# Kernel optimization log

Hardware: AMD Instinct MI355X
Metric: run time of the kernel (lower is better)

## Reference

```python
import jax, jax.numpy as jnp
import numpy as np

DIM = 768
N_HEADS = 12
HEAD_DIM = DIM // N_HEADS
MLP_DIM = 3072
DEPTH = 12
B, N = 16, 512


def setup_inputs() -> dict:
    key = jax.random.key(0)
    ks = jax.random.split(key, 12)
    s = 0.02
    return {
        "x": jax.random.normal(ks[0], (B, N, DIM), dtype=jnp.float32),
        "ln_w": jnp.ones((DIM,), jnp.float32),
        "ln_b": jnp.zeros((DIM,), jnp.float32),
        "wq": jax.random.normal(ks[1], (DIM, DIM), jnp.float32) * s,
        "bq": jnp.zeros((DIM,), jnp.float32),
        "wk": jax.random.normal(ks[2], (DIM, DIM), jnp.float32) * s,
        "bk": jnp.zeros((DIM,), jnp.float32),
        "wv": jax.random.normal(ks[3], (DIM, DIM), jnp.float32) * s,
        "bv": jnp.zeros((DIM,), jnp.float32),
        "w1": jax.random.normal(ks[4], (DIM, MLP_DIM), jnp.float32) * s,
        "b1": jnp.zeros((MLP_DIM,), jnp.float32),
        "w2": jax.random.normal(ks[5], (MLP_DIM, DIM), jnp.float32) * s,
        "b2": jnp.zeros((DIM,), jnp.float32),
    }


def _layernorm(x, w, b):
    mu = jnp.mean(x, axis=-1, keepdims=True)
    var = jnp.var(x, axis=-1, keepdims=True)
    return (x - mu) * jax.lax.rsqrt(var + 1e-5) * w + b


def _mha(x, wq, bq, wk, bk, wv, bv):
    # x: [b, n, dim]; weights stored as [in, out]
    def heads(t):
        return t.reshape(B, N, N_HEADS, HEAD_DIM).transpose(0, 2, 1, 3)  # b h n d
    q = heads(x @ wq + bq)
    k = heads(x @ wk + bk)
    v = heads(x @ wv + bv)
    scores = jnp.einsum('bhqd,bhkd->bhqk', q, k) / np.sqrt(HEAD_DIM).astype(np.float32)
    attn = jax.nn.softmax(scores, axis=-1)
    o = jnp.einsum('bhqk,bhkd->bhqd', attn, v)
    return o.transpose(0, 2, 1, 3).reshape(B, N, DIM)


def reference(x, ln_w, ln_b, wq, bq, wk, bk, wv, bv, w1, b1, w2, b2):
    # Dropout is identity in eval mode. Same weights reused each depth iteration.
    for _ in range(DEPTH):
        x = _mha(_layernorm(x, ln_w, ln_b), wq, bq, wk, bk, wv, bv) + x
        h = _layernorm(x, ln_w, ln_b)
        h = jax.nn.gelu(h @ w1 + b1, approximate=False) @ w2 + b2
        x = h + x
    return x
```

## Files before the change

kernel.cpp:

```cpp
#include <hip/hip_runtime.h>

typedef __bf16 bf16x8 __attribute__((ext_vector_type(8)));
typedef float f32x4 __attribute__((ext_vector_type(4)));
typedef unsigned short ushort8_t __attribute__((ext_vector_type(8)));
typedef unsigned short ushort4_t __attribute__((ext_vector_type(4)));

#define MFMA16(a, b, c) __builtin_amdgcn_mfma_f32_16x16x32_bf16((a), (b), (c), 0, 0, 0)

#define GLOAD16(gp, lp)                                                        \
  __builtin_amdgcn_global_load_lds(                                            \
      (__attribute__((address_space(1))) void*)(gp),                           \
      (__attribute__((address_space(3))) void*)(lp), 16, 0, 0)

__device__ __forceinline__ unsigned short f2bf(float f) {
  unsigned u = __builtin_bit_cast(unsigned, f);
  return (unsigned short)((u + 0x7FFFu + ((u >> 16) & 1u)) >> 16);
}


__global__ __launch_bounds__(256) void transpose_f2b_tiled(
    const float* __restrict__ src, unsigned short* __restrict__ dst,
    int Kdim, int Ndim) {
  const long u = (long)blockIdx.x * 256 + threadIdx.x;
  const long total = ((long)Kdim * Ndim) >> 3;
  if (u >= total) return;
  const int kt32 = Kdim >> 5;
  const long tile = u >> 6;
  const int t8 = (int)(u & 63);
  const int chunk = t8 >> 4, rowlow = t8 & 15;
  const int n = (int)(tile / kt32) * 16 + rowlow;
  const int k0 = (int)(tile % kt32) * 32 + chunk * 8;
  ushort8_t o;
#pragma unroll
  for (int e = 0; e < 8; e++) o[e] = f2bf(src[(long)(k0 + e) * Ndim + n]);
  *(ushort8_t*)(dst + (u << 3)) = o;
}

__global__ __launch_bounds__(256) void ln_kernel(
    const float* __restrict__ x, const float* __restrict__ gw,
    const float* __restrict__ gb, unsigned short* __restrict__ h) {
  const int row = blockIdx.x * 4 + (threadIdx.x >> 6);
  const int l = threadIdx.x & 63;
  const float* xr = x + (long)row * 768;
  f32x4 va[3];
#pragma unroll
  for (int i = 0; i < 3; i++) va[i] = *(const f32x4*)(xr + i * 256 + l * 4);
  float s = 0.f, ss = 0.f;
#pragma unroll
  for (int i = 0; i < 3; i++)
#pragma unroll
    for (int j = 0; j < 4; j++) {
      float t = va[i][j];
      s += t;
      ss += t * t;
    }
#pragma unroll
  for (int off = 1; off < 64; off <<= 1) {
    s += __shfl_xor(s, off, 64);
    ss += __shfl_xor(ss, off, 64);
  }
  const float mu = s * (1.f / 768.f);
  const float var = ss * (1.f / 768.f) - mu * mu;
  const float inv = rsqrtf(var + 1e-5f);
  const long tb = ((long)(row >> 4) * 24) << 9;
  const int rlow = (row & 15) * 8;
  const int coff = ((l >> 1) & 3) * 128 + rlow + (l & 1) * 4;
#pragma unroll
  for (int i = 0; i < 3; i++) {
    f32x4 wv = *(const f32x4*)(gw + i * 256 + l * 4);
    f32x4 bv = *(const f32x4*)(gb + i * 256 + l * 4);
    ushort4_t o;
#pragma unroll
    for (int j = 0; j < 4; j++) o[j] = f2bf((va[i][j] - mu) * inv * wv[j] + bv[j]);
    const long addr = tb + ((long)(i * 8 + (l >> 3)) << 9) + coff;
    *(ushort4_t*)(h + addr) = o;
  }
}

enum { EPI_QKV = 0, EPI_GELU = 1, EPI_RES = 2 };

template <int EPI, int MREP>
__global__ __launch_bounds__(256) void gemm_bt(
    const unsigned short* __restrict__ A, const unsigned short* __restrict__ BT,
    int K, const float* __restrict__ bb0, const float* __restrict__ bb1,
    const float* __restrict__ bb2, unsigned short* __restrict__ o0,
    unsigned short* __restrict__ o1, unsigned short* __restrict__ o2,
    const float* oFin, float* oFout) {
  constexpr int BM = MREP * 32;
  constexpr int AG = BM / 16;
  __shared__ unsigned short As[2][2][AG * 512];
  __shared__ unsigned short Bs[2][2][8 * 512];
  const int tid = threadIdx.x;
  const int w = tid >> 6, l = tid & 63;
  const int lr = l & 15, lg = l >> 4;
  const int wr = w >> 1, wc = w & 1;

  const int nx = gridDim.x;
  const int nwg = nx * gridDim.y;
  int wg = blockIdx.y * nx + blockIdx.x;
  {
    const int qq = nwg >> 3, rr = nwg & 7;
    const int xcd = wg & 7, idx = wg >> 3;
    wg = (xcd < rr ? xcd * (qq + 1) : rr * (qq + 1) + (xcd - rr) * qq) + idx;
  }
  const int bx = wg % nx, by = wg / nx;
  const int m0 = by * BM, n0 = bx * 128;

  const int nk32 = K >> 5;
  const long abase = (long)(m0 >> 4) * nk32;
  const long bbase = (long)(n0 >> 4) * nk32;

  auto stage = [&](int buf, int kt) {
#pragma unroll
    for (int kk = 0; kk < 2; kk++) {
      const int pk = kt * 2 + kk;
#pragma unroll
      for (int t = 0; t < AG / 4; t++) {
        const int g = w + t * 4;
        GLOAD16(A + ((abase + (long)g * nk32 + pk) << 9) + l * 8,
                &As[buf][kk][g * 512 + l * 8]);
      }
#pragma unroll
      for (int t = 0; t < 2; t++) {
        const int g = w + t * 4;
        GLOAD16(BT + ((bbase + (long)g * nk32 + pk) << 9) + l * 8,
                &Bs[buf][kk][g * 512 + l * 8]);
      }
    }
  };

  f32x4 acc[MREP][4] = {};
  const int nk = K >> 6;
  stage(0, 0);
  for (int kt = 0; kt < nk; ++kt) {
    const int cur = kt & 1;
    __syncthreads();
    if (kt + 1 < nk) stage(cur ^ 1, kt + 1);
#pragma unroll
    for (int kk = 0; kk < 2; kk++) {
      bf16x8 a[MREP], b[4];
#pragma unroll
      for (int i = 0; i < MREP; i++)
        a[i] = *(const bf16x8*)(&As[cur][kk][(wr * MREP + i) * 512 + l * 8]);
#pragma unroll
      for (int j = 0; j < 4; j++)
        b[j] = *(const bf16x8*)(&Bs[cur][kk][(wc * 4 + j) * 512 + l * 8]);
      __builtin_amdgcn_s_setprio(1);
#pragma unroll
      for (int i = 0; i < MREP; i++)
#pragma unroll
        for (int j = 0; j < 4; j++) acc[i][j] = MFMA16(a[i], b[j], acc[i][j]);
      __builtin_amdgcn_s_setprio(0);
    }
  }

  if (EPI == EPI_QKV) {
    const int whichq = n0 / 768;
    const int cc0 = n0 - whichq * 768;
    const float* bias = whichq == 0 ? bb0 : whichq == 1 ? bb1 : bb2;
    if (whichq < 2) {
      unsigned short* dst = whichq == 0 ? o0 : o1;
#pragma unroll
      for (int i = 0; i < MREP; i++) {
        const int r = m0 + wr * MREP * 16 + i * 16 + lg * 4;
#pragma unroll
        for (int j = 0; j < 4; j++) {
          const int ccol = cc0 + wc * 64 + j * 16 + lr;
          const int hd = ccol >> 6, d = ccol & 63;
          const float bv = bias[ccol];
#pragma unroll
          for (int q = 0; q < 4; q++) {
            const int row = r + q;
            const int bidx = row >> 9, n = row & 511;
            const long addr = ((long)(bidx * 12 + hd) * 512 + n) * 64 + d;
            dst[addr] = f2bf(acc[i][j][q] + bv);
          }
        }
      }
    } else {
#pragma unroll
      for (int i = 0; i < MREP; i++) {
        const int r = m0 + wr * MREP * 16 + i * 16 + lg * 4;
        const int bidx = r >> 9, nb = r & 511;
#pragma unroll
        for (int j = 0; j < 4; j++) {
          const int ccol = cc0 + wc * 64 + j * 16 + lr;
          const int hd = ccol >> 6, d = ccol & 63;
          const float bv = bias[ccol];
          ushort4_t pk;
#pragma unroll
          for (int q = 0; q < 4; q++) pk[q] = f2bf(acc[i][j][q] + bv);
          *(ushort4_t*)(&o2[((long)(bidx * 12 + hd) * 64 + d) * 512 + nb]) = pk;
        }
      }
    }
  } else if (EPI == EPI_GELU) {
#pragma unroll
    for (int i = 0; i < MREP; i++) {
      const int r = m0 + wr * MREP * 16 + i * 16 + lg * 4;
#pragma unroll
      for (int j = 0; j < 4; j++) {
        const int c = n0 + wc * 64 + j * 16 + lr;
        const float bv = bb0[c];
        const long cpart = ((long)(c >> 5) << 9) + ((c >> 3) & 3) * 128 + (c & 7);
#pragma unroll
        for (int q = 0; q < 4; q++) {
          const int row = r + q;
          float v = acc[i][j][q] + bv;
          const float u = v * (0.7978845608f + 0.0356774081f * v * v);
          const float g = v / (1.0f + __expf(-2.0f * u));
          o0[(((long)(row >> 4) * 96) << 9) + cpart + (row & 15) * 8] = f2bf(g);
        }
      }
    }
  } else {
#pragma unroll
    for (int i = 0; i < MREP; i++) {
      const int r = m0 + wr * MREP * 16 + i * 16 + lg * 4;
#pragma unroll
      for (int j = 0; j < 4; j++) {
        const int c = n0 + wc * 64 + j * 16 + lr;
        const float bv = bb0[c];
#pragma unroll
        for (int q = 0; q < 4; q++) {
          const long addr = (long)(r + q) * 768 + c;
          oFout[addr] = acc[i][j][q] + bv + oFin[addr];
        }
      }
    }
  }
}

__global__ __launch_bounds__(256) void attn_kernel(
    const unsigned short* __restrict__ qg, const unsigned short* __restrict__ kg,
    const unsigned short* __restrict__ vtg, float* __restrict__ x) {
  __shared__ unsigned short Sh[128 * 64];
  __shared__ unsigned short Ks[2][64 * 64];
  __shared__ unsigned short Vt[2][64 * 64];
  const int qt = blockIdx.x, h = blockIdx.y, b = blockIdx.z;
  const int bh = b * 12 + h;
  const int tid = threadIdx.x, w = tid >> 6, l = tid & 63;
  const int lr = l & 15, lg = l >> 4;
  const int fchunk = ((l & 7) ^ ((l >> 3) & 7)) * 8;
  const int rk = lr & 7;

  const unsigned short* qbase =
      qg + ((long)bh * 512 + qt * 128 + w * 32 + (l >> 3)) * 64 + fchunk;
  unsigned short* shW = &Sh[w * 2048 + l * 8];
#pragma unroll
  for (int cc = 0; cc < 4; cc++) GLOAD16(qbase + cc * 8 * 64, shW + cc * 512);

  const unsigned short* kbase =
      kg + ((long)bh * 512 + w * 16 + (l >> 3)) * 64 + fchunk;
  const unsigned short* vbase =
      vtg + ((long)bh * 64 + w * 16 + (l >> 3)) * 512 + fchunk;
  unsigned short* KsW = &Ks[0][w * 1024 + l * 8];
  unsigned short* VtW = &Vt[0][w * 1024 + l * 8];

  auto stageKV = [&](int buf, int kt) {
#pragma unroll
    for (int cc = 0; cc < 2; cc++) {
      GLOAD16(kbase + (kt * 64 + cc * 8) * 64, KsW + buf * 4096 + cc * 512);
      GLOAD16(vbase + cc * 8 * 512 + kt * 64, VtW + buf * 4096 + cc * 512);
    }
  };
  stageKV(0, 0);
  __syncthreads();

  bf16x8 qa[2][2];
#pragma unroll
  for (int mi = 0; mi < 2; mi++)
#pragma unroll
    for (int ds = 0; ds < 2; ds++) {
      qa[mi][ds] = *(const bf16x8*)(&Sh[(w * 32 + mi * 16 + lr) * 64 +
                                        ((ds * 4 + lg) ^ rk) * 8]);
#pragma unroll
      for (int e = 0; e < 8; e++)
        qa[mi][ds][e] = (__bf16)(0.125f * (float)qa[mi][ds][e]);
    }

  unsigned short* Pw = &Sh[w * 2048];
  float lsum[8] = {};
  f32x4 o[2][4] = {};

  for (int kt = 0; kt < 8; ++kt) {
    const int cur = kt & 1;
    if (kt < 7) stageKV(cur ^ 1, kt + 1);

    f32x4 s[2][4] = {};
#pragma unroll
    for (int ds = 0; ds < 2; ++ds) {
      bf16x8 kb[4];
#pragma unroll
      for (int nj = 0; nj < 4; nj++)
        kb[nj] = *(const bf16x8*)(&Ks[cur][(nj * 16 + lr) * 64 +
                                           ((ds * 4 + lg) ^ rk) * 8]);
#pragma unroll
      for (int mi = 0; mi < 2; mi++)
#pragma unroll
        for (int nj = 0; nj < 4; nj++) s[mi][nj] = MFMA16(qa[mi][ds], kb[nj], s[mi][nj]);
    }

#pragma unroll
    for (int mi = 0; mi < 2; mi++)
#pragma unroll
      for (int nj = 0; nj < 4; nj++) {
        const int cL = nj * 2 + (lr >> 3);
#pragma unroll
        for (int q = 0; q < 4; q++) {
          const int row = mi * 16 + lg * 4 + q;
          const float p = __expf(s[mi][nj][q]);
          lsum[mi * 4 + q] += p;
          Pw[row * 64 + ((cL ^ (row & 7)) * 8) + (lr & 7)] = f2bf(p);
        }
      }

#pragma unroll
    for (int ks = 0; ks < 2; ++ks) {
      bf16x8 pa[2], vb[4];
#pragma unroll
      for (int mi = 0; mi < 2; mi++)
        pa[mi] = *(const bf16x8*)(&Pw[(mi * 16 + lr) * 64 +
                                      ((ks * 4 + lg) ^ rk) * 8]);
#pragma unroll
      for (int dj = 0; dj < 4; dj++)
        vb[dj] = *(const bf16x8*)(&Vt[cur][(dj * 16 + lr) * 64 +
                                           ((ks * 4 + lg) ^ rk) * 8]);
#pragma unroll
      for (int mi = 0; mi < 2; mi++)
#pragma unroll
        for (int dj = 0; dj < 4; dj++) o[mi][dj] = MFMA16(pa[mi], vb[dj], o[mi][dj]);
    }
    __syncthreads();
  }

#pragma unroll
  for (int i = 0; i < 8; i++) {
#pragma unroll
    for (int off = 1; off < 16; off <<= 1) lsum[i] += __shfl_xor(lsum[i], off, 64);
  }

#pragma unroll
  for (int mi = 0; mi < 2; mi++) {
#pragma unroll
    for (int q = 0; q < 4; q++) {
      const int n = qt * 128 + w * 32 + mi * 16 + lg * 4 + q;
      const float inv = 1.0f / lsum[mi * 4 + q];
      const long base = ((long)(b * 512 + n)) * 768 + h * 64;
#pragma unroll
      for (int dj = 0; dj < 4; dj++) {
        const long a = base + dj * 16 + lr;
        x[a] = x[a] + o[mi][dj][q] * inv;
      }
    }
  }
}

extern "C" void kernel_launch(void* const* d_in, const int* in_sizes, int n_in,
                              void* d_out, int out_size, void* d_ws,
                              size_t ws_size, hipStream_t stream) {
  const float* x_in = (const float*)d_in[0];
  const float* ln_w = (const float*)d_in[1];
  const float* ln_b = (const float*)d_in[2];
  const float* wq = (const float*)d_in[3];
  const float* bq = (const float*)d_in[4];
  const float* wk = (const float*)d_in[5];
  const float* bk = (const float*)d_in[6];
  const float* wv = (const float*)d_in[7];
  const float* bv = (const float*)d_in[8];
  const float* w1 = (const float*)d_in[9];
  const float* b1 = (const float*)d_in[10];
  const float* w2 = (const float*)d_in[11];
  const float* b2 = (const float*)d_in[12];

  char* p = (char*)d_ws;
  float* xw = (float*)p;            p += 8192L * 768 * 4;
  unsigned short* hbuf = (unsigned short*)p;  p += 8192L * 768 * 2;
  unsigned short* wqkvT = (unsigned short*)p; p += 2304L * 768 * 2;
  unsigned short* w1T = (unsigned short*)p;   p += 3072L * 768 * 2;
  unsigned short* w2T = (unsigned short*)p;   p += 768L * 3072 * 2;
  unsigned short* qb = (unsigned short*)p;
  unsigned short* kb = qb + 6291456L;
  unsigned short* vt = kb + 6291456L;
  unsigned short* gbuf = qb;

  hipMemcpyAsync(xw, x_in, 8192L * 768 * 4, hipMemcpyDeviceToDevice, stream);

  transpose_f2b_tiled<<<(768 * 768 / 8 + 255) / 256, 256, 0, stream>>>(
      wq, wqkvT, 768, 768);
  transpose_f2b_tiled<<<(768 * 768 / 8 + 255) / 256, 256, 0, stream>>>(
      wk, wqkvT + 768L * 768, 768, 768);
  transpose_f2b_tiled<<<(768 * 768 / 8 + 255) / 256, 256, 0, stream>>>(
      wv, wqkvT + 2L * 768 * 768, 768, 768);
  transpose_f2b_tiled<<<(768 * 3072 / 8 + 255) / 256, 256, 0, stream>>>(
      w1, w1T, 768, 3072);
  transpose_f2b_tiled<<<(768 * 3072 / 8 + 255) / 256, 256, 0, stream>>>(
      w2, w2T, 3072, 768);

  for (int layer = 0; layer < 12; ++layer) {
    ln_kernel<<<2048, 256, 0, stream>>>(xw, ln_w, ln_b, hbuf);
    gemm_bt<EPI_QKV, 4><<<dim3(18, 64), 256, 0, stream>>>(
        hbuf, wqkvT, 768, bq, bk, bv, qb, kb, vt, nullptr, nullptr);
    attn_kernel<<<dim3(4, 12, 16), 256, 0, stream>>>(qb, kb, vt, xw);
    ln_kernel<<<2048, 256, 0, stream>>>(xw, ln_w, ln_b, hbuf);
    gemm_bt<EPI_GELU, 4><<<dim3(24, 64), 256, 0, stream>>>(
        hbuf, w1T, 768, b1, nullptr, nullptr, gbuf, nullptr, nullptr, nullptr,
        nullptr);
    gemm_bt<EPI_RES, 2><<<dim3(6, 128), 256, 0, stream>>>(
        gbuf, w2T, 3072, b2, nullptr, nullptr, nullptr, nullptr, nullptr, xw,
        layer == 11 ? (float*)d_out : xw);
  }
}
```

Baseline: 2.493 ms.

## Use a 256x256-tile, 512-thread double-buffered GEMM for the MLP up-projection

Adds a new GEMM kernel with 256x256 output tiles, 8 waves per block and double-buffered LDS staging loaded directly from global memory. It uses explicit vmcnt waits, scheduling fences, MFMA priority boosts and an XCD-aware remapping of workgroup IDs. The GELU+bias epilogue writes bf16 in the existing tiled layout. The kernel replaces the smaller-tile gemm_bt for the w1 GEMM to raise data reuse per loaded tile. The trade-off is that the grid is only 384 large blocks with about 128KB of LDS each, so only one block fits per CU and the last wave may leave CUs idle.

Result: slower. 2.596 ms (+4.1%).

```diff
diff --git a/kernel.cpp b/kernel.cpp
--- a/kernel.cpp
+++ b/kernel.cpp
@@ -11,6 +11,9 @@
   __builtin_amdgcn_global_load_lds(                                            \
       (__attribute__((address_space(1))) void*)(gp),                           \
       (__attribute__((address_space(3))) void*)(lp), 16, 0, 0)
+
+#define WAITVM(N) asm volatile("s_waitcnt vmcnt(" #N ")" ::: "memory")
+#define SCHEDFENCE __builtin_amdgcn_sched_barrier(0)
 
 __device__ __forceinline__ unsigned short f2bf(float f) {
   unsigned u = __builtin_bit_cast(unsigned, f);
@@ -78,6 +81,100 @@
 }
 
 enum { EPI_QKV = 0, EPI_GELU = 1, EPI_RES = 2 };
+
+template <int EPI>
+__global__ __launch_bounds__(512) void gemm256p(
+    const unsigned short* __restrict__ A, const unsigned short* __restrict__ BT,
+    int K, const float* __restrict__ bb0, unsigned short* __restrict__ o0) {
+  __shared__ unsigned short As[2][2][8192];
+  __shared__ unsigned short Bs[2][2][8192];
+  const int tid = threadIdx.x;
+  const int w = tid >> 6, l = tid & 63;
+  const int lr = l & 15, lg = l >> 4;
+  const int wr = w >> 2, wc = w & 3;
+
+  const int nx = gridDim.x;
+  const int nwg = nx * gridDim.y;
+  int wg = blockIdx.y * nx + blockIdx.x;
+  {
+    const int qq = nwg >> 3, rr = nwg & 7;
+    const int xcd = wg & 7, idx = wg >> 3;
+    wg = (xcd < rr ? xcd * (qq + 1) : rr * (qq + 1) + (xcd - rr) * qq) + idx;
+  }
+  const int bx = wg % nx, by = wg / nx;
+  const int m0 = by * 256, n0 = bx * 256;
+
+  const int nk32 = K >> 5;
+  const long abase = (long)(m0 >> 4) * nk32;
+  const long bbase = (long)(n0 >> 4) * nk32;
+
+  auto stage = [&](int t) {
+    const int slot = t & 1;
+#pragma unroll
+    for (int kk = 0; kk < 2; kk++) {
+      const int pk = t * 2 + kk;
+      GLOAD16(A + ((abase + (long)w * nk32 + pk) << 9) + l * 8,
+              &As[slot][kk][w * 512 + l * 8]);
+      GLOAD16(A + ((abase + (long)(w + 8) * nk32 + pk) << 9) + l * 8,
+              &As[slot][kk][(w + 8) * 512 + l * 8]);
+      GLOAD16(BT + ((bbase + (long)w * nk32 + pk) << 9) + l * 8,
+              &Bs[slot][kk][w * 512 + l * 8]);
+      GLOAD16(BT + ((bbase + (long)(w + 8) * nk32 + pk) << 9) + l * 8,
+              &Bs[slot][kk][(w + 8) * 512 + l * 8]);
+    }
+  };
+
+  f32x4 acc[8][4] = {};
+  const int nk = K >> 6;
+  stage(0);
+  stage(1);
+  for (int t = 0; t < nk; ++t) {
+    const int slot = t & 1;
+    if (t + 1 < nk) { WAITVM(8); } else { WAITVM(0); }
+    SCHEDFENCE;
+    __builtin_amdgcn_s_barrier();
+    SCHEDFENCE;
+#pragma unroll
+    for (int kk = 0; kk < 2; kk++) {
+      bf16x8 a[8], b[4];
+#pragma unroll
+      for (int i = 0; i < 8; i++)
+        a[i] = *(const bf16x8*)(&As[slot][kk][(wr * 8 + i) * 512 + l * 8]);
+#pragma unroll
+      for (int j = 0; j < 4; j++)
+        b[j] = *(const bf16x8*)(&Bs[slot][kk][(wc * 4 + j) * 512 + l * 8]);
+      __builtin_amdgcn_s_setprio(1);
+#pragma unroll
+      for (int i = 0; i < 8; i++)
+#pragma unroll
+        for (int j = 0; j < 4; j++) acc[i][j] = MFMA16(a[i], b[j], acc[i][j]);
+      __builtin_amdgcn_s_setprio(0);
+    }
+    SCHEDFENCE;
+    __builtin_amdgcn_s_barrier();
+    SCHEDFENCE;
+    if (t + 2 < nk) stage(t + 2);
+  }
+
+#pragma unroll
+  for (int fm = 0; fm < 8; fm++) {
+    const int r = m0 + wr * 128 + fm * 16 + lg * 4;
+#pragma unroll
+    for (int fn = 0; fn < 4; fn++) {
+      const int c = n0 + wc * 64 + fn * 16 + lr;
+      const float bv = bb0[c];
+      const long cpart = ((long)(c >> 5) << 9) + ((c >> 3) & 3) * 128 + (c & 7);
+#pragma unroll
+      for (int q = 0; q < 4; q++) {
+        const int row = r + q;
+        float v = acc[fm][fn][q] + bv;
+        const float u = v * (0.7978845608f + 0.0356774081f * v * v);
+        const float g = v / (1.0f + __expf(-2.0f * u));
+        o0[(((long)(row >> 4) * 96) << 9) + cpart + (row & 15) * 8] = f2bf(g);
+      }
+    }
+  }
+}
 
 template <int EPI, int MREP>
 __global__ __launch_bounds__(256) void gemm_bt(
@@ -403,9 +500,8 @@
         hbuf, wqkvT, 768, bq, bk, bv, qb, kb, vt, nullptr, nullptr);
     attn_kernel<<<dim3(4, 12, 16), 256, 0, stream>>>(qb, kb, vt, xw);
     ln_kernel<<<2048, 256, 0, stream>>>(xw, ln_w, ln_b, hbuf);
-    gemm_bt<EPI_GELU, 4><<<dim3(24, 64), 256, 0, stream>>>(
-        hbuf, w1T, 768, b1, nullptr, nullptr, gbuf, nullptr, nullptr, nullptr,
-        nullptr);
+    gemm256p<EPI_GELU><<<dim3(12, 32), 512, 0, stream>>>(
+        hbuf, w1T, 768, b1, gbuf);
     gemm_bt<EPI_RES, 2><<<dim3(6, 128), 256, 0, stream>>>(
         gbuf, w2T, 3072, b2, nullptr, nullptr, nullptr, nullptr, nullptr, xw,
         layer == 11 ? (float*)d_out : xw);
```
